# Optimization experiments

Hardware: AMD Instinct MI355X
Metric: run time of the kernel (lower is better)

The kernel has to match this reference:

```python
import jax, jax.numpy as jnp
import numpy as np

N = 160000
K = 16
C_IN = 64
C_OUT = 128
C_MID = 16  # weightnet out


def _lin_bn(x, W, g, b):
    # Linear (no bias) followed by eval-mode BatchNorm folded into per-channel affine
    return (x @ W) * g + b


def _lrelu(x):
    return jnp.where(x > 0, x, 0.1 * x)


def setup_inputs() -> dict:
    key = jax.random.key(0)
    ks = jax.random.split(key, 12)
    d = {}
    d['dense_xyz'] = jax.random.normal(ks[0], (1, N, 3), dtype=jnp.float32)
    d['dense_feats'] = jax.random.normal(ks[1], (1, N, C_IN), dtype=jnp.float32)
    d['nei_inds'] = jax.random.randint(ks[2], (1, N, K), 0, N, dtype=jnp.int32)
    def lin(k, fan_in, fan_out):
        return jax.random.normal(k, (fan_in, fan_out), dtype=jnp.float32) / np.sqrt(fan_in)
    d['W_u1'] = lin(ks[3], C_IN, C_OUT // 4)
    d['g_u1'] = jnp.ones((C_OUT // 4,), jnp.float32); d['b_u1'] = jnp.zeros((C_OUT // 4,), jnp.float32)
    d['W_wn0'] = lin(ks[4], 3, 8); d['g_wn0'] = jnp.ones((8,), jnp.float32); d['b_wn0'] = jnp.zeros((8,), jnp.float32)
    d['W_wn1'] = lin(ks[5], 8, 8); d['g_wn1'] = jnp.ones((8,), jnp.float32); d['b_wn1'] = jnp.zeros((8,), jnp.float32)
    d['W_wn2'] = lin(ks[6], 8, C_MID); d['g_wn2'] = jnp.ones((C_MID,), jnp.float32); d['b_wn2'] = jnp.zeros((C_MID,), jnp.float32)
    d['W_lin'] = lin(ks[7], (C_OUT // 4) * C_MID, C_OUT // 2)
    d['g_lin'] = jnp.ones((C_OUT // 2,), jnp.float32); d['b_lin'] = jnp.zeros((C_OUT // 2,), jnp.float32)
    d['W_u2'] = lin(ks[8], C_OUT // 2, C_OUT)
    d['g_u2'] = jnp.ones((C_OUT,), jnp.float32); d['b_u2'] = jnp.zeros((C_OUT,), jnp.float32)
    d['W_sc'] = lin(ks[9], C_IN, C_OUT)
    d['g_sc'] = jnp.ones((C_OUT,), jnp.float32); d['b_sc'] = jnp.zeros((C_OUT,), jnp.float32)
    return d


def reference(dense_xyz, dense_feats, nei_inds,
              W_u1, g_u1, b_u1,
              W_wn0, g_wn0, b_wn0,
              W_wn1, g_wn1, b_wn1,
              W_wn2, g_wn2, b_wn2,
              W_lin, g_lin, b_lin,
              W_u2, g_u2, b_u2,
              W_sc, g_sc, b_sc):
    B, n, _ = dense_xyz.shape
    gather = jax.vmap(lambda tbl, idx: tbl[idx])  # (n,c),(n,k)->(n,k,c), vmapped over batch

    # unary1: Linear+BN+LeakyReLU(0.1)
    feats_x = _lrelu(_lin_bn(dense_feats, W_u1, g_u1, b_u1))  # [B,N,32]

    gathered_xyz = gather(dense_xyz, nei_inds)                 # [B,N,K,3]
    localized_xyz = gathered_xyz - dense_xyz[:, :, None, :]    # [B,N,K,3]

    w = jax.nn.relu(_lin_bn(localized_xyz, W_wn0, g_wn0, b_wn0))
    w = jax.nn.relu(_lin_bn(w, W_wn1, g_wn1, b_wn1))
    w = jax.nn.relu(_lin_bn(w, W_wn2, g_wn2, b_wn2))           # [B,N,K,16]

    gathered_feat = gather(feats_x, nei_inds)                  # [B,N,K,32]
    # PointConv aggregation: per-point (C x K) @ (K x C_mid)
    new_feat = jnp.einsum('bnkc,bnkw->bncw', gathered_feat, w).reshape(B, n, -1)  # [B,N,512]

    new_feat = jax.nn.relu(_lin_bn(new_feat, W_lin, g_lin, b_lin))  # [B,N,64]
    new_feat = _lin_bn(new_feat, W_u2, g_u2, b_u2)                  # [B,N,128], no relu

    shortcut = _lin_bn(dense_feats, W_sc, g_sc, b_sc)               # [B,N,128]
    out = _lrelu(new_feat + shortcut)
    return out, localized_xyz
```

## Files before the change

kernel.cpp:

```cpp
#include <hip/hip_runtime.h>
#include <stdint.h>

typedef unsigned short u16;
typedef unsigned int   u32;

typedef __attribute__((ext_vector_type(8))) short bf16x8;
typedef __attribute__((ext_vector_type(4))) float f32x4;


__device__ __forceinline__ float bf2f(u16 h) {
  return __uint_as_float(((u32)h) << 16);
}
__device__ __forceinline__ float lrelu(float x) { return x > 0.f ? x : 0.1f * x; }

__device__ __forceinline__ float ldf(const void* p, size_t i, bool bf) {
  return bf ? bf2f(((const u16*)p)[i]) : ((const float*)p)[i];
}
__device__ __forceinline__ bool probe_bf16(const void* g) {
  return ((*(const u32*)g) & 0xFFFFu) == 0x3F80u;
}
__device__ __forceinline__ u16 f2bf(float x) {
  u32 u = __float_as_uint(x);
  return (u16)((u + 0x7FFFu + ((u >> 16) & 1u)) >> 16);
}

__global__ __launch_bounds__(256) void k1_unary(
    const void* __restrict__ feats, const void* __restrict__ W,
    const void* __restrict__ g, const void* __restrict__ b,
    u16* __restrict__ fx, int Npts)
{
  __shared__ float sW[64 * 32];
  __shared__ float sb[32];
  __shared__ float sf[8][64];
  bool bf = probe_bf16(g);
  int tid = threadIdx.x;
  for (int e = tid; e < 2048; e += 256) sW[e] = ldf(W, e, bf) * ldf(g, e & 31, bf);
  if (tid < 32) sb[tid] = ldf(b, tid, bf);
  int n0 = blockIdx.x * 8;
  for (int e = tid; e < 512; e += 256) {
    int p = e >> 6, i = e & 63;
    int n = n0 + p;
    sf[p][i] = (n < Npts) ? ldf(feats, (size_t)n * 64 + i, bf) : 0.f;
  }
  __syncthreads();
  int p = tid >> 5, c = tid & 31;
  int n = n0 + p;
  if (n < Npts) {
    float acc = sb[c];
#pragma unroll
    for (int i = 0; i < 64; ++i) acc += sf[p][i] * sW[i * 32 + c];
    fx[(size_t)n * 32 + c] = f2bf(lrelu(acc));
  }
}

__global__ __launch_bounds__(256) void k2_point(
    const void* __restrict__ xyz, const int* __restrict__ nei,
    const u16* __restrict__ fx,
    const void* __restrict__ W0, const void* __restrict__ g0, const void* __restrict__ b0,
    const void* __restrict__ W1, const void* __restrict__ g1, const void* __restrict__ b1,
    const void* __restrict__ W2, const void* __restrict__ g2, const void* __restrict__ b2,
    u16* __restrict__ nf16, float* __restrict__ locout, int n0, int n1)
{
  __shared__ float sW0[24], sB0[8], sW1[64], sB1[8], sW2[128], sB2[16];
  __shared__ int   sIdx[4][16];
  __shared__ float sLoc[4][48];
  __shared__ float sHa[4][128];
  __shared__ float sHb[4][128];
  alignas(16) __shared__ u16 sPT[4][16 * 24];
  alignas(16) __shared__ u16 sGFT[4][32 * 24];

  bool bf = probe_bf16(g0);
  int tid = threadIdx.x;
  if (tid < 24) sW0[tid] = ldf(W0, tid, bf) * ldf(g0, tid & 7, bf);
  else if (tid < 32) sB0[tid - 24] = ldf(b0, tid - 24, bf);
  else if (tid < 96) sW1[tid - 32] = ldf(W1, tid - 32, bf) * ldf(g1, (tid - 32) & 7, bf);
  else if (tid < 104) sB1[tid - 96] = ldf(b1, tid - 96, bf);
  else if (tid < 232) sW2[tid - 104] = ldf(W2, tid - 104, bf) * ldf(g2, (tid - 104) & 15, bf);
  else if (tid < 248) sB2[tid - 232] = ldf(b2, tid - 232, bf);

  int w = tid >> 6, lane = tid & 63;
  int n = n0 + blockIdx.x * 4 + w;
  bool valid = n < n1;

  if (lane < 16) sIdx[w][lane] = valid ? nei[(size_t)n * 16 + lane] : 0;
  __syncthreads();

  if (lane < 48) {
    int k = lane / 3, d = lane - k * 3;
    float v = 0.f;
    if (valid) {
      int m = sIdx[w][k];
      v = ldf(xyz, (size_t)m * 3 + d, bf) - ldf(xyz, (size_t)n * 3 + d, bf);
      locout[(size_t)n * 48 + lane] = v;
    }
    sLoc[w][lane] = v;
  }

  {
    int k = lane & 15, cg = lane >> 4;
    int m = sIdx[w][k];
    bf16x8 v = *reinterpret_cast<const bf16x8*>(fx + (size_t)m * 32 + cg * 8);
#pragma unroll
    for (int e = 0; e < 8; ++e)
      sGFT[w][(cg * 8 + e) * 24 + k] = (u16)v[e];
  }
  __syncthreads();

#pragma unroll
  for (int r = 0; r < 2; ++r) {
    int o = lane + r * 64;
    int k = o >> 3, j = o & 7;
    float a = sB0[j];
#pragma unroll
    for (int d = 0; d < 3; ++d) a += sLoc[w][k * 3 + d] * sW0[d * 8 + j];
    sHa[w][o] = fmaxf(a, 0.f);
  }
  __syncthreads();
#pragma unroll
  for (int r = 0; r < 2; ++r) {
    int o = lane + r * 64;
    int k = o >> 3, j = o & 7;
    float a = sB1[j];
#pragma unroll
    for (int d = 0; d < 8; ++d) a += sHa[w][k * 8 + d] * sW1[d * 8 + j];
    sHb[w][o] = fmaxf(a, 0.f);
  }
  __syncthreads();
#pragma unroll
  for (int r = 0; r < 4; ++r) {
    int o = lane + r * 64;
    int k = o >> 4, j = o & 15;
    float a = sB2[j];
#pragma unroll
    for (int d = 0; d < 8; ++d) a += sHb[w][k * 8 + d] * sW2[d * 16 + j];
    sPT[w][j * 24 + k] = f2bf(fmaxf(a, 0.f));
  }
  __syncthreads();

  {
    int kgrp = lane >> 4;
    int cb = lane & 15;
    bf16x8 a0 = (bf16x8){0,0,0,0,0,0,0,0};
    bf16x8 a1 = a0, b = a0;
    if (kgrp < 2) {
      a0 = *reinterpret_cast<const bf16x8*>(&sGFT[w][(cb)      * 24 + kgrp * 8]);
      a1 = *reinterpret_cast<const bf16x8*>(&sGFT[w][(16 + cb) * 24 + kgrp * 8]);
      b  = *reinterpret_cast<const bf16x8*>(&sPT [w][(cb)      * 24 + kgrp * 8]);
    }
    f32x4 acc0 = (f32x4){0.f, 0.f, 0.f, 0.f};
    f32x4 acc1 = acc0;
    acc0 = __builtin_amdgcn_mfma_f32_16x16x32_bf16(a0, b, acc0, 0, 0, 0);
    acc1 = __builtin_amdgcn_mfma_f32_16x16x32_bf16(a1, b, acc1, 0, 0, 0);
    if (valid) {
      u16* dst = nf16 + (size_t)(n - n0) * 512;
      int rq = lane >> 4;
#pragma unroll
      for (int v = 0; v < 4; ++v) {
        int c0 = rq * 4 + v;
        int c1 = 16 + rq * 4 + v;
        dst[c0 * 16 + cb] = f2bf(acc0[v]);
        dst[c1 * 16 + cb] = f2bf(acc1[v]);
      }
    }
  }
}

__global__ __launch_bounds__(256) void k3_gemm(
    const u16* __restrict__ nf, const void* __restrict__ WL,
    const void* __restrict__ gl, const void* __restrict__ bl,
    u16* __restrict__ h, int cnt)
{
  alignas(16) __shared__ u16 As[128 * 64];
  alignas(16) __shared__ u16 Bs[64 * 512];
  bool bf = probe_bf16(gl);
  int t = threadIdx.x;
  int lane = t & 63, w = t >> 6;
  int m0 = blockIdx.x * 128;

  {
    int c = t & 63, kh = t >> 6;
    float gc = ldf(gl, c, bf);
    int k0 = kh * 128;
#pragma unroll
    for (int q = 0; q < 16; ++q) {
      int kbase = k0 + q * 8;
      bf16x8 pk;
#pragma unroll
      for (int e = 0; e < 8; ++e)
        pk[e] = (short)f2bf(ldf(WL, (size_t)(kbase + e) * 64 + c, bf) * gc);
      int chunk = (kbase >> 3) ^ (c & 7);
      *reinterpret_cast<bf16x8*>(&Bs[c * 512 + chunk * 8]) = pk;
    }
  }

  f32x4 acc[2][4];
#pragma unroll
  for (int mi = 0; mi < 2; ++mi)
#pragma unroll
    for (int ni = 0; ni < 4; ++ni) acc[mi][ni] = (f32x4){0.f, 0.f, 0.f, 0.f};

  int mrow = t >> 1;
  int half = t & 1;

  for (int kb = 0; kb < 512; kb += 64) {
    __syncthreads();
    {
      int gm = m0 + mrow;
      if (gm >= cnt) gm = cnt - 1;
      const u16* src = nf + (size_t)gm * 512 + kb + half * 32;
#pragma unroll
      for (int q = 0; q < 4; ++q) {
        bf16x8 v = *reinterpret_cast<const bf16x8*>(src + q * 8);
        int chunk = (half * 4 + q) ^ (mrow & 7);
        *reinterpret_cast<bf16x8*>(&As[mrow * 64 + chunk * 8]) = v;
      }
    }
    __syncthreads();
#pragma unroll
    for (int ks = 0; ks < 2; ++ks) {
      int qg = lane >> 4;
      bf16x8 a[2];
#pragma unroll
      for (int mi = 0; mi < 2; ++mi) {
        int row = w * 32 + mi * 16 + (lane & 15);
        int chunk = (ks * 4 + qg) ^ (row & 7);
        a[mi] = *reinterpret_cast<const bf16x8*>(&As[row * 64 + chunk * 8]);
      }
      bf16x8 bfr[4];
#pragma unroll
      for (int ni = 0; ni < 4; ++ni) {
        int col = ni * 16 + (lane & 15);
        int chunk = ((kb >> 3) + ks * 4 + qg) ^ (col & 7);
        bfr[ni] = *reinterpret_cast<const bf16x8*>(&Bs[col * 512 + chunk * 8]);
      }
#pragma unroll
      for (int mi = 0; mi < 2; ++mi)
#pragma unroll
        for (int ni = 0; ni < 4; ++ni)
          acc[mi][ni] = __builtin_amdgcn_mfma_f32_16x16x32_bf16(
              a[mi], bfr[ni], acc[mi][ni], 0, 0, 0);
    }
  }

  int colb = lane & 15, rq = lane >> 4;
  float bias[4];
#pragma unroll
  for (int ni = 0; ni < 4; ++ni) bias[ni] = ldf(bl, ni * 16 + colb, bf);
#pragma unroll
  for (int mi = 0; mi < 2; ++mi) {
#pragma unroll
    for (int v = 0; v < 4; ++v) {
      int m = m0 + w * 32 + mi * 16 + rq * 4 + v;
      if (m < cnt) {
#pragma unroll
        for (int ni = 0; ni < 4; ++ni) {
          int j = ni * 16 + colb;
          h[(size_t)m * 64 + j] = f2bf(fmaxf(acc[mi][ni][v] + bias[ni], 0.f));
        }
      }
    }
  }
}

__global__ __launch_bounds__(256) void k4_gemm(
    const u16* __restrict__ hb, const void* __restrict__ feats,
    const void* __restrict__ Wu2, const void* __restrict__ gu2, const void* __restrict__ bu2,
    const void* __restrict__ Wsc, const void* __restrict__ gsc, const void* __restrict__ bsc,
    float* __restrict__ out, int n0c, int cnt)
{
  alignas(16) __shared__ u16 As[128 * 128];
  alignas(16) __shared__ u16 Bs[128 * 128];
  bool bf = probe_bf16(gu2);
  int t = threadIdx.x;
  int lane = t & 63, w = t >> 6;
  int m0 = blockIdx.x * 128;

  {
    int c = t & 127, kh = t >> 7;
    const void* Wsel = kh ? Wsc : Wu2;
    const void* gsel = kh ? gsc : gu2;
    float gc = ldf(gsel, c, bf);
#pragma unroll
    for (int q = 0; q < 8; ++q) {
      bf16x8 pk;
#pragma unroll
      for (int e = 0; e < 8; ++e)
        pk[e] = (short)f2bf(ldf(Wsel, (size_t)(q * 8 + e) * 128 + c, bf) * gc);
      int chunk = (kh * 8 + q) ^ (c & 7);
      *reinterpret_cast<bf16x8*>(&Bs[c * 128 + chunk * 8]) = pk;
    }
  }
  {
    int r = t >> 1, half = t & 1;
    int gm = m0 + r;
    if (gm >= cnt) gm = cnt - 1;
    if (half == 0) {
      const u16* src = hb + (size_t)gm * 64;
#pragma unroll
      for (int q = 0; q < 8; ++q) {
        bf16x8 v = *reinterpret_cast<const bf16x8*>(src + q * 8);
        int chunk = q ^ (r & 7);
        *reinterpret_cast<bf16x8*>(&As[r * 128 + chunk * 8]) = v;
      }
    } else if (bf) {
      const u16* src = (const u16*)feats + (size_t)(n0c + gm) * 64;
#pragma unroll
      for (int q = 0; q < 8; ++q) {
        bf16x8 v = *reinterpret_cast<const bf16x8*>(src + q * 8);
        int chunk = (8 + q) ^ (r & 7);
        *reinterpret_cast<bf16x8*>(&As[r * 128 + chunk * 8]) = v;
      }
    } else {
      const float* src = (const float*)feats + (size_t)(n0c + gm) * 64;
#pragma unroll
      for (int q = 0; q < 8; ++q) {
        bf16x8 pk;
#pragma unroll
        for (int e = 0; e < 8; ++e) pk[e] = (short)f2bf(src[q * 8 + e]);
        int chunk = (8 + q) ^ (r & 7);
        *reinterpret_cast<bf16x8*>(&As[r * 128 + chunk * 8]) = pk;
      }
    }
  }
  __syncthreads();

  f32x4 acc[2][8];
#pragma unroll
  for (int mi = 0; mi < 2; ++mi)
#pragma unroll
    for (int ni = 0; ni < 8; ++ni) acc[mi][ni] = (f32x4){0.f, 0.f, 0.f, 0.f};

  int qg = lane >> 4;
#pragma unroll
  for (int ks = 0; ks < 4; ++ks) {
    bf16x8 a[2];
#pragma unroll
    for (int mi = 0; mi < 2; ++mi) {
      int row = w * 32 + mi * 16 + (lane & 15);
      int chunk = (ks * 4 + qg) ^ (row & 7);
      a[mi] = *reinterpret_cast<const bf16x8*>(&As[row * 128 + chunk * 8]);
    }
#pragma unroll
    for (int ni = 0; ni < 8; ++ni) {
      int col = ni * 16 + (lane & 15);
      int chunk = (ks * 4 + qg) ^ (col & 7);
      bf16x8 b = *reinterpret_cast<const bf16x8*>(&Bs[col * 128 + chunk * 8]);
      acc[0][ni] = __builtin_amdgcn_mfma_f32_16x16x32_bf16(a[0], b, acc[0][ni], 0, 0, 0);
      acc[1][ni] = __builtin_amdgcn_mfma_f32_16x16x32_bf16(a[1], b, acc[1][ni], 0, 0, 0);
    }
  }

  int colb = lane & 15, rq = lane >> 4;
  float bias[8];
#pragma unroll
  for (int ni = 0; ni < 8; ++ni) {
    int c = ni * 16 + colb;
    bias[ni] = ldf(bu2, c, bf) + ldf(bsc, c, bf);
  }
#pragma unroll
  for (int mi = 0; mi < 2; ++mi) {
#pragma unroll
    for (int v = 0; v < 4; ++v) {
      int m = m0 + w * 32 + mi * 16 + rq * 4 + v;
      if (m < cnt) {
        float* orow = out + (size_t)(n0c + m) * 128;
#pragma unroll
        for (int ni = 0; ni < 8; ++ni)
          orow[ni * 16 + colb] = lrelu(acc[mi][ni][v] + bias[ni]);
      }
    }
  }
}

extern "C" void kernel_launch(void* const* d_in, const int* in_sizes, int n_in,
                              void* d_out, int out_size, void* d_ws, size_t ws_size,
                              hipStream_t stream) {
  const void* xyz   = d_in[0];
  const void* feats = d_in[1];
  const int*  nei   = (const int*)d_in[2];
  const void* W_u1  = d_in[3];
  const void* g_u1  = d_in[4];
  const void* b_u1  = d_in[5];
  const void* W_wn0 = d_in[6];
  const void* g_wn0 = d_in[7];
  const void* b_wn0 = d_in[8];
  const void* W_wn1 = d_in[9];
  const void* g_wn1 = d_in[10];
  const void* b_wn1 = d_in[11];
  const void* W_wn2 = d_in[12];
  const void* g_wn2 = d_in[13];
  const void* b_wn2 = d_in[14];
  const void* W_lin = d_in[15];
  const void* g_lin = d_in[16];
  const void* b_lin = d_in[17];
  const void* W_u2  = d_in[18];
  const void* g_u2  = d_in[19];
  const void* b_u2  = d_in[20];
  const void* W_sc  = d_in[21];
  const void* g_sc  = d_in[22];
  const void* b_sc  = d_in[23];

  int Npts = in_sizes[0] / 3;

  float* out0 = (float*)d_out;
  float* out1 = out0 + (size_t)Npts * 128;

  u16* fx = (u16*)d_ws;
  size_t fx_bytes = (size_t)Npts * 32 * 2;
  size_t avail = (ws_size > fx_bytes) ? (ws_size - fx_bytes) : 0;
  size_t per_pt = (size_t)512 * 2 + (size_t)64 * 2;
  long long cN = (long long)(avail / per_pt);
  if (cN < 1) cN = 1;
  if (cN > Npts) cN = Npts;
  int chunkN = (int)cN;

  u16* nf16 = fx + (size_t)Npts * 32;
  u16* hb   = nf16 + (size_t)chunkN * 512;

  k1_unary<<<(Npts + 7) / 8, 256, 0, stream>>>(feats, W_u1, g_u1, b_u1, fx, Npts);

  for (int n0 = 0; n0 < Npts; n0 += chunkN) {
    int n1 = n0 + chunkN;
    if (n1 > Npts) n1 = Npts;
    int cnt = n1 - n0;
    k2_point<<<(cnt + 3) / 4, 256, 0, stream>>>(
        xyz, nei, fx,
        W_wn0, g_wn0, b_wn0, W_wn1, g_wn1, b_wn1, W_wn2, g_wn2, b_wn2,
        nf16, out1, n0, n1);
    k3_gemm<<<(cnt + 127) / 128, 256, 0, stream>>>(nf16, W_lin, g_lin, b_lin, hb, cnt);
    k4_gemm<<<(cnt + 127) / 128, 256, 0, stream>>>(hb, feats, W_u2, g_u2, b_u2,
                                                   W_sc, g_sc, b_sc, out0, n0, cnt);
  }
}
```

Baseline: 444.1 us.

## Use MFMA for unary1 GEMM and vectorize transposed nf16 stores

```diff
diff --git a/kernel.cpp b/kernel.cpp
--- a/kernel.cpp
+++ b/kernel.cpp
@@ -5,6 +5,7 @@
 typedef unsigned int   u32;
 
 typedef __attribute__((ext_vector_type(8))) short bf16x8;
+typedef __attribute__((ext_vector_type(4))) short bf16x4;
 typedef __attribute__((ext_vector_type(4))) float f32x4;
 
 
@@ -29,27 +30,87 @@
     const void* __restrict__ g, const void* __restrict__ b,
     u16* __restrict__ fx, int Npts)
 {
-  __shared__ float sW[64 * 32];
-  __shared__ float sb[32];
-  __shared__ float sf[8][64];
+  alignas(16) __shared__ u16 As[128 * 64];
+  alignas(16) __shared__ u16 Bs[32 * 64];
   bool bf = probe_bf16(g);
-  int tid = threadIdx.x;
-  for (int e = tid; e < 2048; e += 256) sW[e] = ldf(W, e, bf) * ldf(g, e & 31, bf);
-  if (tid < 32) sb[tid] = ldf(b, tid, bf);
-  int n0 = blockIdx.x * 8;
-  for (int e = tid; e < 512; e += 256) {
-    int p = e >> 6, i = e & 63;
-    int n = n0 + p;
-    sf[p][i] = (n < Npts) ? ldf(feats, (size_t)n * 64 + i, bf) : 0.f;
-  }
-  __syncthreads();
-  int p = tid >> 5, c = tid & 31;
-  int n = n0 + p;
-  if (n < Npts) {
-    float acc = sb[c];
-#pragma unroll
-    for (int i = 0; i < 64; ++i) acc += sf[p][i] * sW[i * 32 + c];
-    fx[(size_t)n * 32 + c] = f2bf(lrelu(acc));
+  int t = threadIdx.x;
+  int lane = t & 63, w = t >> 6;
+  int m0 = blockIdx.x * 128;
+
+  {
+    int c = t & 31, kh = t >> 5;
+    float gc = ldf(g, c, bf);
+    bf16x8 pk;
+#pragma unroll
+    for (int e = 0; e < 8; ++e)
+      pk[e] = (short)f2bf(ldf(W, (size_t)(kh * 8 + e) * 32 + c, bf) * gc);
+    int chunk = kh ^ (c & 7);
+    *reinterpret_cast<bf16x8*>(&Bs[c * 64 + chunk * 8]) = pk;
+  }
+  {
+    int r = t >> 1, half = t & 1;
+    int gm = m0 + r;
+    if (gm >= Npts) gm = Npts - 1;
+    if (bf) {
+      const u16* src = (const u16*)feats + (size_t)gm * 64 + half * 32;
+#pragma unroll
+      for (int q = 0; q < 4; ++q) {
+        bf16x8 v = *reinterpret_cast<const bf16x8*>(src + q * 8);
+        int chunk = (half * 4 + q) ^ (r & 7);
+        *reinterpret_cast<bf16x8*>(&As[r * 64 + chunk * 8]) = v;
+      }
+    } else {
+      const float* src = (const float*)feats + (size_t)gm * 64 + half * 32;
+#pragma unroll
+      for (int q = 0; q < 4; ++q) {
+        bf16x8 pk;
+#pragma unroll
+        for (int e = 0; e < 8; ++e) pk[e] = (short)f2bf(src[q * 8 + e]);
+        int chunk = (half * 4 + q) ^ (r & 7);
+        *reinterpret_cast<bf16x8*>(&As[r * 64 + chunk * 8]) = pk;
+      }
+    }
+  }
+  __syncthreads();
+
+  f32x4 acc[2][2];
+#pragma unroll
+  for (int mi = 0; mi < 2; ++mi)
+#pragma unroll
+    for (int ni = 0; ni < 2; ++ni) acc[mi][ni] = (f32x4){0.f, 0.f, 0.f, 0.f};
+
+  int qg = lane >> 4, cb = lane & 15;
+#pragma unroll
+  for (int ks = 0; ks < 2; ++ks) {
+    bf16x8 a[2];
+#pragma unroll
+    for (int mi = 0; mi < 2; ++mi) {
+      int row = w * 32 + mi * 16 + cb;
+      int chunk = (ks * 4 + qg) ^ (row & 7);
+      a[mi] = *reinterpret_cast<const bf16x8*>(&As[row * 64 + chunk * 8]);
+    }
+#pragma unroll
+    for (int ni = 0; ni < 2; ++ni) {
+      int col = ni * 16 + cb;
+      int chunk = (ks * 4 + qg) ^ (col & 7);
+      bf16x8 bv = *reinterpret_cast<const bf16x8*>(&Bs[col * 64 + chunk * 8]);
+      acc[0][ni] = __builtin_amdgcn_mfma_f32_16x16x32_bf16(a[0], bv, acc[0][ni], 0, 0, 0);
+      acc[1][ni] = __builtin_amdgcn_mfma_f32_16x16x32_bf16(a[1], bv, acc[1][ni], 0, 0, 0);
+    }
+  }
+
+  int rq = lane >> 4;
+  float bias[2] = {ldf(b, cb, bf), ldf(b, 16 + cb, bf)};
+#pragma unroll
+  for (int mi = 0; mi < 2; ++mi) {
+#pragma unroll
+    for (int v = 0; v < 4; ++v) {
+      int m = m0 + w * 32 + mi * 16 + rq * 4 + v;
+      if (m < Npts) {
+        fx[(size_t)m * 32 + cb]      = f2bf(lrelu(acc[mi][0][v] + bias[0]));
+        fx[(size_t)m * 32 + 16 + cb] = f2bf(lrelu(acc[mi][1][v] + bias[1]));
+      }
+    }
   }
 }
 
@@ -154,13 +215,11 @@
     if (valid) {
       u16* dst = nf16 + (size_t)(n - n0) * 512;
       int rq = lane >> 4;
-#pragma unroll
-      for (int v = 0; v < 4; ++v) {
-        int c0 = rq * 4 + v;
-        int c1 = 16 + rq * 4 + v;
-        dst[c0 * 16 + cb] = f2bf(acc0[v]);
-        dst[c1 * 16 + cb] = f2bf(acc1[v]);
-      }
+      bf16x4 p0, p1;
+#pragma unroll
+      for (int v = 0; v < 4; ++v) { p0[v] = (short)f2bf(acc0[v]); p1[v] = (short)f2bf(acc1[v]); }
+      *reinterpret_cast<bf16x4*>(dst + cb * 32 + rq * 4)      = p0;
+      *reinterpret_cast<bf16x4*>(dst + cb * 32 + 16 + rq * 4) = p1;
     }
   }
 }
@@ -186,8 +245,12 @@
       int kbase = k0 + q * 8;
       bf16x8 pk;
 #pragma unroll
-      for (int e = 0; e < 8; ++e)
-        pk[e] = (short)f2bf(ldf(WL, (size_t)(kbase + e) * 64 + c, bf) * gc);
+      for (int e = 0; e < 8; ++e) {
+        int kp = kbase + e;
+        int j = kp >> 5, cc = kp & 31;
+        int krow = cc * 16 + j;
+        pk[e] = (short)f2bf(ldf(WL, (size_t)krow * 64 + c, bf) * gc);
+      }
       int chunk = (kbase >> 3) ^ (c & 7);
       *reinterpret_cast<bf16x8*>(&Bs[c * 512 + chunk * 8]) = pk;
     }
@@ -417,7 +480,7 @@
   u16* nf16 = fx + (size_t)Npts * 32;
   u16* hb   = nf16 + (size_t)chunkN * 512;
 
-  k1_unary<<<(Npts + 7) / 8, 256, 0, stream>>>(feats, W_u1, g_u1, b_u1, fx, Npts);
+  k1_unary<<<(Npts + 127) / 128, 256, 0, stream>>>(feats, W_u1, g_u1, b_u1, fx, Npts);
 
   for (int n0 = 0; n0 < Npts; n0 += chunkN) {
     int n1 = n0 + chunkN;
```

New measurement: 399.1 us. -10.1%, faster.
